# Optimization experiments

Hardware: AMD Instinct MI355X
Metric: run time of the kernel (lower is better)

Reference implementation:

```python
import jax, jax.numpy as jnp
import numpy as np

N_ATOMS = 1_000_000
DESC_DIM = 128
HIDDEN = 128
N_ELEM = 4  # element ids 0..3


def setup_inputs() -> dict:
    key = jax.random.key(0)
    ks = jax.random.split(key, 6)
    element = jax.random.randint(ks[0], (N_ATOMS,), 0, N_ELEM, dtype=jnp.int32)
    desc = jax.random.normal(ks[1], (N_ATOMS, DESC_DIM), dtype=jnp.float32)
    # Per-element MLP experts: desc_dim -> hidden -> 1
    W1 = jax.random.normal(ks[2], (N_ELEM, DESC_DIM, HIDDEN), dtype=jnp.float32) / np.sqrt(DESC_DIM)
    b1 = jnp.zeros((N_ELEM, HIDDEN), dtype=jnp.float32)
    W2 = jax.random.normal(ks[3], (N_ELEM, HIDDEN), dtype=jnp.float32) / np.sqrt(HIDDEN)
    b2 = jnp.zeros((N_ELEM,), dtype=jnp.float32)
    return {"element": element, "desc": desc, "W1": W1, "b1": b1, "W2": W2, "b2": b2}


def reference(element, desc, W1, b1, W2, b2):
    """Per-element dispatch: each atom's descriptor goes through the MLP for
    its atomic number. JAX jit needs static shapes, so we compute each
    expert densely and select with where (loop over small fixed expert set)."""
    out = jnp.zeros(desc.shape[0], dtype=desc.dtype)
    for e in range(W1.shape[0]):
        h = jax.nn.relu(desc @ W1[e] + b1[e])      # [N, HIDDEN]
        y = h @ W2[e] + b2[e]                       # [N]
        out = jnp.where(element == e, y, out)
    return out
```

## Files before the change

kernel.cpp:

```cpp
#include <hip/hip_runtime.h>
#include <hip/hip_bf16.h>

typedef __attribute__((ext_vector_type(8))) short short8;
typedef __attribute__((ext_vector_type(4))) float float4v;

__device__ __forceinline__ unsigned short f2bf(float f) {
    unsigned int u = __float_as_uint(f);
    u += 0x7fffu + ((u >> 16) & 1u);
    return (unsigned short)(u >> 16);
}

__global__ void count_kernel(const int* __restrict__ elem, int n, int* __restrict__ bc) {
    const int t = threadIdx.x, b = blockIdx.x;
    const int base = b * 1024;
    int c[4] = {0, 0, 0, 0};
    #pragma unroll
    for (int i = 0; i < 4; ++i) {
        const int a = base + i * 256 + t;
        if (a < n) c[elem[a]]++;
    }
    int p0 = c[0] | (c[1] << 16);
    int p1 = c[2] | (c[3] << 16);
    #pragma unroll
    for (int off = 1; off < 64; off <<= 1) { p0 += __shfl_xor(p0, off); p1 += __shfl_xor(p1, off); }
    __shared__ int wsum[4][4];
    const int w = t >> 6, lane = t & 63;
    if (lane == 0) {
        wsum[w][0] = p0 & 0xffff; wsum[w][1] = p0 >> 16;
        wsum[w][2] = p1 & 0xffff; wsum[w][3] = p1 >> 16;
    }
    __syncthreads();
    if (t < 4) {
        int s = 0;
        #pragma unroll
        for (int ww = 0; ww < 4; ++ww) s += wsum[ww][t];
        bc[b * 4 + t] = s;
    }
}

__global__ void scan_kernel(int* __restrict__ bc, int* __restrict__ offs, int nb) {
    const int t = threadIdx.x, w = t >> 6, lane = t & 63;
    int vals[16];
    int s = 0;
    #pragma unroll
    for (int j = 0; j < 16; ++j) {
        const int i = lane * 16 + j;
        const int v = (i < nb) ? bc[i * 4 + w] : 0;
        vals[j] = s; s += v;
    }
    int incl = s;
    #pragma unroll
    for (int off = 1; off < 64; off <<= 1) {
        const int v = __shfl_up(incl, off);
        if (lane >= off) incl += v;
    }
    const int excl = incl - s;
    __shared__ int tot[4];
    __shared__ int eoff[4];
    if (lane == 63) tot[w] = incl;
    __syncthreads();
    if (t == 0) {
        int a = 0;
        for (int e = 0; e < 4; ++e) { eoff[e] = a; offs[e] = a; a += tot[e]; }
        offs[4] = a;
    }
    __syncthreads();
    const int myoff = eoff[w] + excl;
    #pragma unroll
    for (int j = 0; j < 16; ++j) {
        const int i = lane * 16 + j;
        if (i < nb) bc[i * 4 + w] = myoff + vals[j];
    }
}

__global__ void scatter_kernel(const int* __restrict__ elem, int n,
                               const int* __restrict__ bc, int* __restrict__ idx_sorted) {
    const int t = threadIdx.x, b = blockIdx.x;
    const int w = t >> 6, lane = t & 63;
    const int base = b * 1024;
    int ev[4];
    #pragma unroll
    for (int i = 0; i < 4; ++i) {
        const int a = base + i * 256 + t;
        ev[i] = (a < n) ? elem[a] : -1;
    }
    __shared__ int tbl[4][4][4];
    __shared__ int sbase[4];
    #pragma unroll
    for (int i = 0; i < 4; ++i) {
        #pragma unroll
        for (int el = 0; el < 4; ++el) {
            const unsigned long long m = __ballot(ev[i] == el);
            if (lane == 0) tbl[i][w][el] = (int)__popcll(m);
        }
    }
    if (t < 4) sbase[t] = bc[b * 4 + t];
    __syncthreads();
    if (t < 4) {
        int s = 0;
        for (int i = 0; i < 4; ++i)
            for (int w2 = 0; w2 < 4; ++w2) { const int v = tbl[i][w2][t]; tbl[i][w2][t] = s; s += v; }
    }
    __syncthreads();
    #pragma unroll
    for (int i = 0; i < 4; ++i) {
        unsigned long long m[4];
        #pragma unroll
        for (int el = 0; el < 4; ++el) m[el] = __ballot(ev[i] == el);
        const int a = base + i * 256 + t;
        if (a < n) {
            const int el = ev[i];
            const int rank = (int)__popcll(m[el] & ((1ull << lane) - 1ull));
            idx_sorted[sbase[el] + tbl[i][w][el] + rank] = a;
        }
    }
}

__global__ void w1t_kernel(const float* __restrict__ W1, unsigned short* __restrict__ W1T) {
    const int b = blockIdx.x;
    const int e = b >> 7, nn = b & 127;
    const int k = threadIdx.x;
    const float v = W1[((size_t)(e * 128 + k)) * 128 + nn];
    W1T[((size_t)(e * 128 + nn)) * 128 + k] = f2bf(v);
}

__global__ __launch_bounds__(256, 3)
void expert_mlp_kernel(const float* __restrict__ desc,
                       const unsigned short* __restrict__ W1T,
                       const float* __restrict__ b1,
                       const float* __restrict__ W2,
                       const float* __restrict__ b2,
                       const int* __restrict__ idx_sorted,
                       const int* __restrict__ offs,
                       float* __restrict__ out) {
    const int bx = blockIdx.x;
    const int e = bx & 3;
    const int tile = bx >> 2;
    const int base = offs[e];
    const int cnt = offs[e + 1] - base;
    const int m0 = tile * 128;
    if (m0 >= cnt) return;

    const int t = threadIdx.x;
    const int lane = t & 63;
    const int wv = t >> 6;
    const int quad = lane >> 4;
    const int l16 = lane & 15;
    const int mbase = wv * 32;

    const int gm0 = m0 + mbase + l16;
    const int gm1 = gm0 + 16;
    const int cl = cnt - 1;
    const int gi0 = idx_sorted[base + (gm0 < cl ? gm0 : cl)];
    const int gi1 = idx_sorted[base + (gm1 < cl ? gm1 : cl)];

    const float* arow0 = desc + (size_t)gi0 * 128 + quad * 8;
    const float* arow1 = desc + (size_t)gi1 * 128 + quad * 8;
    const unsigned short* brow = W1T + (size_t)e * 16384 + l16 * 128 + quad * 8;

    float4v acc[2][8] = {};
    #pragma unroll
    for (int ks = 0; ks < 4; ++ks) {
        const float4 fa0 = *(const float4*)(arow0 + ks * 32);
        const float4 fb0 = *(const float4*)(arow0 + ks * 32 + 4);
        const float4 fa1 = *(const float4*)(arow1 + ks * 32);
        const float4 fb1 = *(const float4*)(arow1 + ks * 32 + 4);
        short8 a0, a1;
        a0[0] = (short)f2bf(fa0.x); a0[1] = (short)f2bf(fa0.y);
        a0[2] = (short)f2bf(fa0.z); a0[3] = (short)f2bf(fa0.w);
        a0[4] = (short)f2bf(fb0.x); a0[5] = (short)f2bf(fb0.y);
        a0[6] = (short)f2bf(fb0.z); a0[7] = (short)f2bf(fb0.w);
        a1[0] = (short)f2bf(fa1.x); a1[1] = (short)f2bf(fa1.y);
        a1[2] = (short)f2bf(fa1.z); a1[3] = (short)f2bf(fa1.w);
        a1[4] = (short)f2bf(fb1.x); a1[5] = (short)f2bf(fb1.y);
        a1[6] = (short)f2bf(fb1.z); a1[7] = (short)f2bf(fb1.w);
        #pragma unroll
        for (int nt = 0; nt < 8; ++nt) {
            const short8 bf = *(const short8*)(brow + nt * 2048 + ks * 32);
            acc[0][nt] = __builtin_amdgcn_mfma_f32_16x16x32_bf16(a0, bf, acc[0][nt], 0, 0, 0);
            acc[1][nt] = __builtin_amdgcn_mfma_f32_16x16x32_bf16(a1, bf, acc[1][nt], 0, 0, 0);
        }
    }

    float b1v[8], w2v[8];
    #pragma unroll
    for (int nt = 0; nt < 8; ++nt) {
        b1v[nt] = b1[e * 128 + nt * 16 + l16];
        w2v[nt] = W2[e * 128 + nt * 16 + l16];
    }
    const float b2e = b2[e];
    #pragma unroll
    for (int mt = 0; mt < 2; ++mt) {
        float y[4] = {0.f, 0.f, 0.f, 0.f};
        #pragma unroll
        for (int nt = 0; nt < 8; ++nt) {
            const float4v v = acc[mt][nt];
            #pragma unroll
            for (int r = 0; r < 4; ++r)
                y[r] += fmaxf(v[r] + b1v[nt], 0.f) * w2v[nt];
        }
        #pragma unroll
        for (int off = 1; off < 16; off <<= 1) {
            #pragma unroll
            for (int r = 0; r < 4; ++r) y[r] += __shfl_xor(y[r], off, 16);
        }
        if (l16 == 0) {
            #pragma unroll
            for (int r = 0; r < 4; ++r) {
                const int m = mbase + mt * 16 + quad * 4 + r;
                const int gm = m0 + m;
                if (gm < cnt) out[idx_sorted[base + gm]] = y[r] + b2e;
            }
        }
    }
}

extern "C" void kernel_launch(void* const* d_in, const int* in_sizes, int n_in,
                              void* d_out, int out_size, void* d_ws, size_t ws_size,
                              hipStream_t stream) {
    const int*   elem = (const int*)d_in[0];
    const float* desc = (const float*)d_in[1];
    const float* W1   = (const float*)d_in[2];
    const float* b1   = (const float*)d_in[3];
    const float* W2   = (const float*)d_in[4];
    const float* b2   = (const float*)d_in[5];
    float* out = (float*)d_out;
    const int n = in_sizes[0];

    char* ws = (char*)d_ws;
    int* bc         = (int*)ws;
    int* offs       = (int*)(ws + 16128);
    int* idx_sorted = (int*)(ws + 16384);
    unsigned short* W1T = (unsigned short*)(ws + 16384 + (size_t)n * 4);

    const int nb = (n + 1023) / 1024;
    count_kernel  <<<nb, 256, 0, stream>>>(elem, n, bc);
    scan_kernel   <<<1, 256, 0, stream>>>(bc, offs, nb);
    scatter_kernel<<<nb, 256, 0, stream>>>(elem, n, bc, idx_sorted);
    w1t_kernel    <<<512, 128, 0, stream>>>(W1, W1T);

    const int tiles = (n + 127) / 128;
    expert_mlp_kernel<<<tiles * 4, 256, 0, stream>>>(desc, W1T, b1, W2, b2, idx_sorted, offs, out);
}
```

Baseline: 779.7 us.

## Stage MFMA-fragment-ordered W1 in LDS and loop persistent blocks over tiles

Reorders the bf16 W1 copy into MFMA fragment order so each block can copy its expert's weights into shared memory once with coalesced 16-byte loads. The MLP kernel becomes persistent, with 512 blocks per expert looping over 128-row tiles and reading B fragments from LDS instead of global or L2 on every tile. This removes repeated weight loads and launches far fewer blocks. In exchange each block uses 32 KB of LDS, which may limit occupancy, and the fixed grid can balance work unevenly when element counts differ.

```diff
diff --git a/kernel.cpp b/kernel.cpp
--- a/kernel.cpp
+++ b/kernel.cpp
@@ -116,71 +116,50 @@
     }
 }
 
-__global__ void w1t_kernel(const float* __restrict__ W1, unsigned short* __restrict__ W1T) {
+__global__ void w1f_kernel(const float* __restrict__ W1, unsigned short* __restrict__ W1F) {
     const int b = blockIdx.x;
-    const int e = b >> 7, nn = b & 127;
-    const int k = threadIdx.x;
-    const float v = W1[((size_t)(e * 128 + k)) * 128 + nn];
-    W1T[((size_t)(e * 128 + nn)) * 128 + k] = f2bf(v);
-}
+    const int e = b >> 3, nt = b & 7;
+    const int t = threadIdx.x;
+    const int ks = t >> 6, l = t & 63;
+    const int quad = l >> 4, l16 = l & 15;
+    const int n = nt * 16 + l16;
+    const int kb = (ks * 4 + quad) * 8;
+    unsigned short* dst = W1F + ((size_t)(e * 32 + nt * 4 + ks) * 64 + l) * 8;
+    #pragma unroll
+    for (int j = 0; j < 8; ++j)
+        dst[j] = f2bf(W1[((size_t)(e * 128 + kb + j)) * 128 + n]);
+}
+
+#define NBPE 512
 
 __global__ __launch_bounds__(256, 3)
 void expert_mlp_kernel(const float* __restrict__ desc,
-                       const unsigned short* __restrict__ W1T,
+                       const unsigned short* __restrict__ W1F,
                        const float* __restrict__ b1,
                        const float* __restrict__ W2,
                        const float* __restrict__ b2,
                        const int* __restrict__ idx_sorted,
                        const int* __restrict__ offs,
                        float* __restrict__ out) {
+    __shared__ unsigned short Bs[32 * 64 * 8];
+
     const int bx = blockIdx.x;
     const int e = bx & 3;
-    const int tile = bx >> 2;
+    const int blk = bx >> 2;
+    const int t = threadIdx.x;
+
+    {
+        const uint4* src = (const uint4*)(W1F + (size_t)e * 16384);
+        uint4* dst = (uint4*)Bs;
+        #pragma unroll
+        for (int p = 0; p < 8; ++p) dst[p * 256 + t] = src[p * 256 + t];
+    }
+
     const int base = offs[e];
-    const int cnt = offs[e + 1] - base;
-    const int m0 = tile * 128;
-    if (m0 >= cnt) return;
-
-    const int t = threadIdx.x;
-    const int lane = t & 63;
-    const int wv = t >> 6;
-    const int quad = lane >> 4;
-    const int l16 = lane & 15;
+    const int cnt  = offs[e + 1] - base;
+    const int lane = t & 63, wv = t >> 6;
+    const int quad = lane >> 4, l16 = lane & 15;
     const int mbase = wv * 32;
-
-    const int gm0 = m0 + mbase + l16;
-    const int gm1 = gm0 + 16;
-    const int cl = cnt - 1;
-    const int gi0 = idx_sorted[base + (gm0 < cl ? gm0 : cl)];
-    const int gi1 = idx_sorted[base + (gm1 < cl ? gm1 : cl)];
-
-    const float* arow0 = desc + (size_t)gi0 * 128 + quad * 8;
-    const float* arow1 = desc + (size_t)gi1 * 128 + quad * 8;
-    const unsigned short* brow = W1T + (size_t)e * 16384 + l16 * 128 + quad * 8;
-
-    float4v acc[2][8] = {};
-    #pragma unroll
-    for (int ks = 0; ks < 4; ++ks) {
-        const float4 fa0 = *(const float4*)(arow0 + ks * 32);
-        const float4 fb0 = *(const float4*)(arow0 + ks * 32 + 4);
-        const float4 fa1 = *(const float4*)(arow1 + ks * 32);
-        const float4 fb1 = *(const float4*)(arow1 + ks * 32 + 4);
-        short8 a0, a1;
-        a0[0] = (short)f2bf(fa0.x); a0[1] = (short)f2bf(fa0.y);
-        a0[2] = (short)f2bf(fa0.z); a0[3] = (short)f2bf(fa0.w);
-        a0[4] = (short)f2bf(fb0.x); a0[5] = (short)f2bf(fb0.y);
-        a0[6] = (short)f2bf(fb0.z); a0[7] = (short)f2bf(fb0.w);
-        a1[0] = (short)f2bf(fa1.x); a1[1] = (short)f2bf(fa1.y);
-        a1[2] = (short)f2bf(fa1.z); a1[3] = (short)f2bf(fa1.w);
-        a1[4] = (short)f2bf(fb1.x); a1[5] = (short)f2bf(fb1.y);
-        a1[6] = (short)f2bf(fb1.z); a1[7] = (short)f2bf(fb1.w);
-        #pragma unroll
-        for (int nt = 0; nt < 8; ++nt) {
-            const short8 bf = *(const short8*)(brow + nt * 2048 + ks * 32);
-            acc[0][nt] = __builtin_amdgcn_mfma_f32_16x16x32_bf16(a0, bf, acc[0][nt], 0, 0, 0);
-            acc[1][nt] = __builtin_amdgcn_mfma_f32_16x16x32_bf16(a1, bf, acc[1][nt], 0, 0, 0);
-        }
-    }
 
     float b1v[8], w2v[8];
     #pragma unroll
@@ -189,27 +168,66 @@
         w2v[nt] = W2[e * 128 + nt * 16 + l16];
     }
     const float b2e = b2[e];
-    #pragma unroll
-    for (int mt = 0; mt < 2; ++mt) {
-        float y[4] = {0.f, 0.f, 0.f, 0.f};
-        #pragma unroll
-        for (int nt = 0; nt < 8; ++nt) {
-            const float4v v = acc[mt][nt];
+
+    __syncthreads();
+
+    const int cl = cnt - 1;
+    for (int tile = blk; tile * 128 < cnt; tile += NBPE) {
+        const int m0 = tile * 128;
+        const int gm0 = m0 + mbase + l16;
+        const int gm1 = gm0 + 16;
+        const int gi0 = idx_sorted[base + (gm0 < cl ? gm0 : cl)];
+        const int gi1 = idx_sorted[base + (gm1 < cl ? gm1 : cl)];
+        const float* arow0 = desc + (size_t)gi0 * 128 + quad * 8;
+        const float* arow1 = desc + (size_t)gi1 * 128 + quad * 8;
+
+        float4v acc[2][8] = {};
+        #pragma unroll
+        for (int ks = 0; ks < 4; ++ks) {
+            const float4 fa0 = *(const float4*)(arow0 + ks * 32);
+            const float4 fb0 = *(const float4*)(arow0 + ks * 32 + 4);
+            const float4 fa1 = *(const float4*)(arow1 + ks * 32);
+            const float4 fb1 = *(const float4*)(arow1 + ks * 32 + 4);
+            short8 a0, a1;
+            a0[0] = (short)f2bf(fa0.x); a0[1] = (short)f2bf(fa0.y);
+            a0[2] = (short)f2bf(fa0.z); a0[3] = (short)f2bf(fa0.w);
+            a0[4] = (short)f2bf(fb0.x); a0[5] = (short)f2bf(fb0.y);
+            a0[6] = (short)f2bf(fb0.z); a0[7] = (short)f2bf(fb0.w);
+            a1[0] = (short)f2bf(fa1.x); a1[1] = (short)f2bf(fa1.y);
+            a1[2] = (short)f2bf(fa1.z); a1[3] = (short)f2bf(fa1.w);
+            a1[4] = (short)f2bf(fb1.x); a1[5] = (short)f2bf(fb1.y);
+            a1[6] = (short)f2bf(fb1.z); a1[7] = (short)f2bf(fb1.w);
+            const short8* bfp = (const short8*)Bs + ks * 64 + lane;
             #pragma unroll
-            for (int r = 0; r < 4; ++r)
-                y[r] += fmaxf(v[r] + b1v[nt], 0.f) * w2v[nt];
-        }
-        #pragma unroll
-        for (int off = 1; off < 16; off <<= 1) {
+            for (int nt = 0; nt < 8; ++nt) {
+                const short8 bf = bfp[nt * 256];
+                acc[0][nt] = __builtin_amdgcn_mfma_f32_16x16x32_bf16(a0, bf, acc[0][nt], 0, 0, 0);
+                acc[1][nt] = __builtin_amdgcn_mfma_f32_16x16x32_bf16(a1, bf, acc[1][nt], 0, 0, 0);
+            }
+        }
+
+        #pragma unroll
+        for (int mt = 0; mt < 2; ++mt) {
+            float y[4] = {0.f, 0.f, 0.f, 0.f};
             #pragma unroll
-            for (int r = 0; r < 4; ++r) y[r] += __shfl_xor(y[r], off, 16);
-        }
-        if (l16 == 0) {
+            for (int nt = 0; nt < 8; ++nt) {
+                const float4v v = acc[mt][nt];
+                #pragma unroll
+                for (int r = 0; r < 4; ++r)
+                    y[r] += fmaxf(v[r] + b1v[nt], 0.f) * w2v[nt];
+            }
             #pragma unroll
-            for (int r = 0; r < 4; ++r) {
-                const int m = mbase + mt * 16 + quad * 4 + r;
-                const int gm = m0 + m;
-                if (gm < cnt) out[idx_sorted[base + gm]] = y[r] + b2e;
+            for (int off = 1; off < 16; off <<= 1) {
+                #pragma unroll
+                for (int r = 0; r < 4; ++r) y[r] += __shfl_xor(y[r], off, 16);
+            }
+            if (l16 == 0) {
+                #pragma unroll
+                for (int r = 0; r < 4; ++r) {
+                    const int m = mbase + mt * 16 + quad * 4 + r;
+                    const int gm = m0 + m;
+                    if (gm < cnt) out[idx_sorted[base + gm]] = y[r] + b2e;
+                }
             }
         }
     }
@@ -231,14 +249,13 @@
     int* bc         = (int*)ws;
     int* offs       = (int*)(ws + 16128);
     int* idx_sorted = (int*)(ws + 16384);
-    unsigned short* W1T = (unsigned short*)(ws + 16384 + (size_t)n * 4);
+    unsigned short* W1F = (unsigned short*)(ws + 16384 + (size_t)n * 4);
 
     const int nb = (n + 1023) / 1024;
     count_kernel  <<<nb, 256, 0, stream>>>(elem, n, bc);
     scan_kernel   <<<1, 256, 0, stream>>>(bc, offs, nb);
     scatter_kernel<<<nb, 256, 0, stream>>>(elem, n, bc, idx_sorted);
-    w1t_kernel    <<<512, 128, 0, stream>>>(W1, W1T);
-
-    const int tiles = (n + 127) / 128;
-    expert_mlp_kernel<<<tiles * 4, 256, 0, stream>>>(desc, W1T, b1, W2, b2, idx_sorted, offs, out);
-}
+    w1f_kernel    <<<32, 256, 0, stream>>>(W1, W1F);
+
+    expert_mlp_kernel<<<4 * NBPE, 256, 0, stream>>>(desc, W1F, b1, W2, b2, idx_sorted, offs, out);
+}
```

Result: slower. 850.6 us (+9.1%).
